# Kernel tuning notes

Measured on AMD Instinct MI355X. Metric: run time of the kernel, lower is better.

## Reference

```python
import jax, jax.numpy as jnp
import numpy as np
import math

N_QUBITS = 6
N_LAYERS = 3
OUT_DIM = 8
B = 131072
F = 24


def _gate_rx(a):
    # RX(a) = [[cos(a/2), -i sin(a/2)], [-i sin(a/2), cos(a/2)]]; a: scalar or [B]
    c = jnp.cos(a / 2).astype(jnp.complex64)
    s = (-1j * jnp.sin(a / 2)).astype(jnp.complex64)
    return jnp.stack([jnp.stack([c, s], -1), jnp.stack([s, c], -1)], -2)


def _gate_ry(a):
    c = jnp.cos(a / 2).astype(jnp.complex64)
    s = jnp.sin(a / 2).astype(jnp.complex64)
    return jnp.stack([jnp.stack([c, -s], -1), jnp.stack([s, c], -1)], -2)


def _gate_rz(a):
    # RZ(a) = diag(e^{-ia/2}, e^{ia/2})
    e = jnp.exp(-0.5j * a.astype(jnp.complex64))
    z = jnp.zeros_like(e)
    return jnp.stack([jnp.stack([e, z], -1), jnp.stack([z, jnp.conj(e)], -1)], -2)


def _apply_1q(state, gate, q, batched):
    # state: [B] + [2]*N_QUBITS ; gate: [2,2] or [B,2,2]
    s = jnp.moveaxis(state, 1 + q, 1)
    if batched:
        out = jnp.einsum('bij,bj...->bi...', gate, s)
    else:
        out = jnp.einsum('ij,bj...->bi...', gate, s)
    return jnp.moveaxis(out, 1, 1 + q)


def _apply_cnot(state, c, t):
    # flip target where control bit == 1
    cax = 1 + c
    s0 = jnp.take(state, 0, axis=cax)
    s1 = jnp.take(state, 1, axis=cax)
    tax = 1 + t if t < c else t  # control axis removed
    s1 = jnp.flip(s1, axis=tax)
    return jnp.stack([s0, s1], axis=cax)


def _circuit(x, theta):
    Bn = x.shape[0]
    # pooling branch of forward: chunks of size ceil(F/n_qubits)=4, mean each
    x_packed = x.reshape(Bn, N_QUBITS, F // N_QUBITS).mean(-1)
    angles = jnp.clip(x_packed, -6.0, 6.0) / 6.0 * math.pi  # [B, n_qubits]

    state = jnp.zeros((Bn,) + (2,) * N_QUBITS, dtype=jnp.complex64)
    state = state.at[(slice(None),) + (0,) * N_QUBITS].set(1.0)

    # angle encoding: RX(a_q), RZ(0.5*a_q) per qubit (batched gates)
    for q in range(N_QUBITS):
        state = _apply_1q(state, _gate_rx(angles[:, q]), q, batched=True)
        state = _apply_1q(state, _gate_rz(0.5 * angles[:, q]), q, batched=True)

    for l in range(N_LAYERS):
        for q in range(N_QUBITS - 1):
            state = _apply_cnot(state, q, q + 1)
        state = _apply_cnot(state, N_QUBITS - 1, 0)
        for q in range(N_QUBITS):
            state = _apply_1q(state, _gate_rx(theta[l, q, 0]), q, batched=False)
            state = _apply_1q(state, _gate_ry(theta[l, q, 1]), q, batched=False)
            state = _apply_1q(state, _gate_rz(theta[l, q, 2]), q, batched=False)

    probs = jnp.abs(state) ** 2  # real
    meas = []
    for k in range(OUT_DIM):
        q = k % N_QUBITS
        if k % 2 == 0:  # PauliZ
            pq = jnp.sum(probs, axis=tuple(a for a in range(1, N_QUBITS + 1) if a != 1 + q))
            meas.append(pq[:, 0] - pq[:, 1])
        else:  # PauliX: Re <psi| X_q |psi>
            flipped = jnp.flip(state, axis=1 + q)
            meas.append(jnp.real(jnp.sum(jnp.conj(state) * flipped, axis=tuple(range(1, N_QUBITS + 1)))))
    return jnp.stack(meas, axis=1).astype(jnp.float32)  # [B, out_dim]


def setup_inputs() -> dict:
    key = jax.random.key(0)
    k1, k2 = jax.random.split(key)
    x = jax.random.normal(k1, (B, F), dtype=jnp.float32)
    theta = jax.random.normal(k2, (N_LAYERS, N_QUBITS, 3), dtype=jnp.float32) * 0.1
    return {"x": x, "theta": theta}


def reference(x, theta):
    return _circuit(x, theta)
```

## Files before the change

### kernel.cpp

```cpp
#include <hip/hip_runtime.h>
#include <math.h>


struct cf { float r, i; };

__device__ __forceinline__ cf cmul(cf a, cf b) {
    return { fmaf(a.r, b.r, -a.i * b.i), fmaf(a.r, b.i, a.i * b.r) };
}
__device__ __forceinline__ cf cmac(cf acc, cf g, cf v) {
    acc.r = fmaf(g.r, v.r, fmaf(-g.i, v.i, acc.r));
    acc.i = fmaf(g.r, v.i, fmaf(g.i, v.r, acc.i));
    return acc;
}

constexpr int DPP_X1  = 0xB1;
constexpr int DPP_X2  = 0x4E;
constexpr int DPP_C01 = 0xB4;

template<int CTRL>
__device__ __forceinline__ float dppf(float v) {
    return __int_as_float(__builtin_amdgcn_mov_dpp(__float_as_int(v), CTRL, 0xF, 0xF, true));
}
template<int CTRL>
__device__ __forceinline__ cf dppc(cf v) { return { dppf<CTRL>(v.r), dppf<CTRL>(v.i) }; }

template<int M>
__device__ __forceinline__ void apply1q(cf* st, cf g00, cf g01, cf g10, cf g11) {
#pragma unroll
    for (int i = 0; i < 16; ++i) {
        if (i & M) continue;
        cf a = st[i], b = st[i + M];
        cf na = cmul(g00, a); na = cmac(na, g01, b);
        cf nb = cmul(g10, a); nb = cmac(nb, g11, b);
        st[i] = na; st[i + M] = nb;
    }
}

template<int XCTRL>
__device__ __forceinline__ void apply1q_lane(cf* st, bool hi, cf g00, cf g01, cf g10, cf g11) {
    cf ga, gb;
    ga.r = hi ? g11.r : g00.r;  ga.i = hi ? g11.i : g00.i;
    gb.r = hi ? g10.r : g01.r;  gb.i = hi ? g10.i : g01.i;
#pragma unroll
    for (int i = 0; i < 16; ++i) {
        cf part = dppc<XCTRL>(st[i]);
        cf n = cmul(ga, st[i]);
        n = cmac(n, gb, part);
        st[i] = n;
    }
}

template<int MC, int MT>
__device__ __forceinline__ void cnot_local(cf* st) {
#pragma unroll
    for (int i = 0; i < 16; ++i) {
        if ((i & MC) && !(i & MT)) { cf t = st[i]; st[i] = st[i + MT]; st[i + MT] = t; }
    }
}

__global__ __launch_bounds__(256, 4) void qsim_kernel(
    const float* __restrict__ x, const float* __restrict__ theta,
    float* __restrict__ out) {
    __shared__ float gs[18 * 8];
    const int t = threadIdx.x;
    if (t < 18) {
        const float* th = theta + t * 3;
        float sx, cx, sy, cy, sz, cz;
        __sincosf(0.5f * th[0], &sx, &cx);
        __sincosf(0.5f * th[1], &sy, &cy);
        __sincosf(0.5f * th[2], &sz, &cz);
        cf m00 = {  cy * cx,  sy * sx };
        cf m01 = { -sy * cx, -cy * sx };
        cf m10 = {  sy * cx, -cy * sx };
        cf m11 = {  cy * cx, -sy * sx };
        cf e0 = { cz, -sz }, e1 = { cz, sz };
        cf g00 = cmul(e0, m00), g01 = cmul(e0, m01);
        cf g10 = cmul(e1, m10), g11 = cmul(e1, m11);
        float* o = gs + t * 8;
        o[0] = g00.r; o[1] = g00.i; o[2] = g01.r; o[3] = g01.i;
        o[4] = g10.r; o[5] = g10.i; o[6] = g11.r; o[7] = g11.i;
    }
    __syncthreads();

    const int g = blockIdx.x * 256 + t;
    const int e = g >> 2;
    const int p = g & 3;
    const bool l1 = (p & 2) != 0;
    const bool l0 = (p & 1) != 0;

    const float4* xv = reinterpret_cast<const float4*>(x + (size_t)e * 24);
    cf v0[6], v1[6];
#pragma unroll
    for (int q = 0; q < 6; ++q) {
        float4 xq = xv[q];
        float m = (xq.x + xq.y + xq.z + xq.w) * 0.25f;
        m = fminf(fmaxf(m, -6.0f), 6.0f);
        float a = m * 0.52359877559829887308f;
        float s2, c2, s4, c4;
        __sincosf(0.50f * a, &s2, &c2);
        __sincosf(0.25f * a, &s4, &c4);
        v0[q] = { c4 * c2, -s4 * c2 };
        v1[q] = { s4 * s2, -c4 * s2 };
    }

    cf f0, f1;
    f0.r = l1 ? v1[0].r : v0[0].r;  f0.i = l1 ? v1[0].i : v0[0].i;
    f1.r = l0 ? v1[1].r : v0[1].r;  f1.i = l0 ? v1[1].i : v0[1].i;

    cf st[16];
    st[0] = cmul(f0, f1);
#pragma unroll
    for (int q = 2; q < 6; ++q) {
        const int m = 8 >> (q - 2);
#pragma unroll
        for (int i = 0; i < 16; i += 2 * m) {
            st[i + m] = cmul(st[i], v1[q]);
            st[i]     = cmul(st[i], v0[q]);
        }
    }

#pragma unroll 1
    for (int l = 0; l < 3; ++l) {
#pragma unroll
        for (int i = 0; i < 16; ++i) st[i] = dppc<DPP_C01>(st[i]);
#pragma unroll
        for (int i = 0; i < 8; ++i) {
            cf lo = st[i], hi = st[i + 8];
            st[i].r     = l0 ? hi.r : lo.r;  st[i].i     = l0 ? hi.i : lo.i;
            st[i + 8].r = l0 ? lo.r : hi.r;  st[i + 8].i = l0 ? lo.i : hi.i;
        }
        cnot_local<8, 4>(st);
        cnot_local<4, 2>(st);
        cnot_local<2, 1>(st);
#pragma unroll
        for (int i = 1; i < 16; i += 2) st[i] = dppc<DPP_X2>(st[i]);

        const float* gg = gs + l * 48;
#define G4(k) cf{gg[8*(k)+0], gg[8*(k)+1]}, cf{gg[8*(k)+2], gg[8*(k)+3]}, \
              cf{gg[8*(k)+4], gg[8*(k)+5]}, cf{gg[8*(k)+6], gg[8*(k)+7]}
        apply1q_lane<DPP_X2>(st, l1, G4(0));
        apply1q_lane<DPP_X1>(st, l0, G4(1));
        apply1q<8>(st, G4(2));
        apply1q<4>(st, G4(3));
        apply1q<2>(st, G4(4));
        apply1q<1>(st, G4(5));
#undef G4
    }

    float z0 = 0.f, z2 = 0.f, z4 = 0.f, x1s = 0.f, x3s = 0.f, x5s = 0.f;
#pragma unroll
    for (int i = 0; i < 16; ++i) {
        float pr = fmaf(st[i].r, st[i].r, st[i].i * st[i].i);
        z0 += pr;
        z2 = (i & 8) ? z2 - pr : z2 + pr;
        z4 = (i & 2) ? z4 - pr : z4 + pr;
        cf part = dppc<DPP_X1>(st[i]);
        x1s = fmaf(st[i].r, part.r, fmaf(st[i].i, part.i, x1s));
    }
    if (l1) z0 = -z0;
#pragma unroll
    for (int i = 0; i < 16; ++i) {
        if (!(i & 4)) x3s = fmaf(st[i].r, st[i + 4].r, fmaf(st[i].i, st[i + 4].i, x3s));
        if (!(i & 1)) x5s = fmaf(st[i].r, st[i + 1].r, fmaf(st[i].i, st[i + 1].i, x5s));
    }
    x3s *= 2.f; x5s *= 2.f;

    z0  += dppf<DPP_X1>(z0);   z0  += dppf<DPP_X2>(z0);
    z2  += dppf<DPP_X1>(z2);   z2  += dppf<DPP_X2>(z2);
    z4  += dppf<DPP_X1>(z4);   z4  += dppf<DPP_X2>(z4);
    x1s += dppf<DPP_X1>(x1s);  x1s += dppf<DPP_X2>(x1s);
    x3s += dppf<DPP_X1>(x3s);  x3s += dppf<DPP_X2>(x3s);
    x5s += dppf<DPP_X1>(x5s);  x5s += dppf<DPP_X2>(x5s);

    float o0 = l1 ? (l0 ? x3s : z2) : (l0 ? x1s : z0);
    float o1 = l1 ? (l0 ? x1s : z0) : (l0 ? x5s : z4);
    out[(size_t)e * 8 + p] = o0;
    out[(size_t)e * 8 + 4 + p] = o1;
}

extern "C" void kernel_launch(void* const* d_in, const int* in_sizes, int n_in,
                              void* d_out, int out_size, void* d_ws, size_t ws_size,
                              hipStream_t stream) {
    const float* x     = (const float*)d_in[0];
    const float* theta = (const float*)d_in[1];
    float* out = (float*)d_out;
    const int B = in_sizes[0] / 24;
    const int threads = B * 4;
    qsim_kernel<<<dim3(threads / 256), dim3(256), 0, stream>>>(x, theta, out);
}
```

Baseline: 89.97 us.

## Precompute circuit unitary in bf16 and apply it per sample with MFMA

```diff
diff --git a/kernel.cpp b/kernel.cpp
--- a/kernel.cpp
+++ b/kernel.cpp
@@ -13,6 +13,9 @@
     return acc;
 }
 
+typedef short short8 __attribute__((ext_vector_type(8)));
+typedef float f32x4 __attribute__((ext_vector_type(4)));
+
 constexpr int DPP_X1  = 0xB1;
 constexpr int DPP_X2  = 0x4E;
 constexpr int DPP_C01 = 0xB4;
@@ -23,6 +26,10 @@
 }
 template<int CTRL>
 __device__ __forceinline__ cf dppc(cf v) { return { dppf<CTRL>(v.r), dppf<CTRL>(v.i) }; }
+
+__device__ __forceinline__ unsigned pkbf(float lo, float hi) {
+    return __builtin_amdgcn_perm(__float_as_uint(hi), __float_as_uint(lo), 0x07060302u);
+}
 
 template<int M>
 __device__ __forceinline__ void apply1q(cf* st, cf g00, cf g01, cf g10, cf g11) {
@@ -35,7 +42,6 @@
         st[i] = na; st[i + M] = nb;
     }
 }
-
 template<int XCTRL>
 __device__ __forceinline__ void apply1q_lane(cf* st, bool hi, cf g00, cf g01, cf g10, cf g11) {
     cf ga, gb;
@@ -49,7 +55,6 @@
         st[i] = n;
     }
 }
-
 template<int MC, int MT>
 __device__ __forceinline__ void cnot_local(cf* st) {
 #pragma unroll
@@ -58,9 +63,8 @@
     }
 }
 
-__global__ __launch_bounds__(256, 4) void qsim_kernel(
-    const float* __restrict__ x, const float* __restrict__ theta,
-    float* __restrict__ out) {
+__global__ void ubuild_kernel(const float* __restrict__ theta,
+                              unsigned short* __restrict__ W) {
     __shared__ float gs[18 * 8];
     const int t = threadIdx.x;
     if (t < 18) {
@@ -82,42 +86,15 @@
     }
     __syncthreads();
 
-    const int g = blockIdx.x * 256 + t;
-    const int e = g >> 2;
-    const int p = g & 3;
+    const int k = t >> 2;
+    const int p = t & 3;
     const bool l1 = (p & 2) != 0;
     const bool l0 = (p & 1) != 0;
 
-    const float4* xv = reinterpret_cast<const float4*>(x + (size_t)e * 24);
-    cf v0[6], v1[6];
-#pragma unroll
-    for (int q = 0; q < 6; ++q) {
-        float4 xq = xv[q];
-        float m = (xq.x + xq.y + xq.z + xq.w) * 0.25f;
-        m = fminf(fmaxf(m, -6.0f), 6.0f);
-        float a = m * 0.52359877559829887308f;
-        float s2, c2, s4, c4;
-        __sincosf(0.50f * a, &s2, &c2);
-        __sincosf(0.25f * a, &s4, &c4);
-        v0[q] = { c4 * c2, -s4 * c2 };
-        v1[q] = { s4 * s2, -c4 * s2 };
-    }
-
-    cf f0, f1;
-    f0.r = l1 ? v1[0].r : v0[0].r;  f0.i = l1 ? v1[0].i : v0[0].i;
-    f1.r = l0 ? v1[1].r : v0[1].r;  f1.i = l0 ? v1[1].i : v0[1].i;
-
     cf st[16];
-    st[0] = cmul(f0, f1);
-#pragma unroll
-    for (int q = 2; q < 6; ++q) {
-        const int m = 8 >> (q - 2);
-#pragma unroll
-        for (int i = 0; i < 16; i += 2 * m) {
-            st[i + m] = cmul(st[i], v1[q]);
-            st[i]     = cmul(st[i], v0[q]);
-        }
-    }
+#pragma unroll
+    for (int i = 0; i < 16; ++i) st[i] = { 0.f, 0.f };
+    if ((k >> 4) == p) st[k & 15] = { 1.f, 0.f };
 
 #pragma unroll 1
     for (int l = 0; l < 3; ++l) {
@@ -136,8 +113,8 @@
         for (int i = 1; i < 16; i += 2) st[i] = dppc<DPP_X2>(st[i]);
 
         const float* gg = gs + l * 48;
-#define G4(k) cf{gg[8*(k)+0], gg[8*(k)+1]}, cf{gg[8*(k)+2], gg[8*(k)+3]}, \
-              cf{gg[8*(k)+4], gg[8*(k)+5]}, cf{gg[8*(k)+6], gg[8*(k)+7]}
+#define G4(kk) cf{gg[8*(kk)+0], gg[8*(kk)+1]}, cf{gg[8*(kk)+2], gg[8*(kk)+3]}, \
+               cf{gg[8*(kk)+4], gg[8*(kk)+5]}, cf{gg[8*(kk)+6], gg[8*(kk)+7]}
         apply1q_lane<DPP_X2>(st, l1, G4(0));
         apply1q_lane<DPP_X1>(st, l0, G4(1));
         apply1q<8>(st, G4(2));
@@ -147,35 +124,152 @@
 #undef G4
     }
 
-    float z0 = 0.f, z2 = 0.f, z4 = 0.f, x1s = 0.f, x3s = 0.f, x5s = 0.f;
-#pragma unroll
-    for (int i = 0; i < 16; ++i) {
-        float pr = fmaf(st[i].r, st[i].r, st[i].i * st[i].i);
-        z0 += pr;
-        z2 = (i & 8) ? z2 - pr : z2 + pr;
-        z4 = (i & 2) ? z4 - pr : z4 + pr;
-        cf part = dppc<DPP_X1>(st[i]);
-        x1s = fmaf(st[i].r, part.r, fmaf(st[i].i, part.i, x1s));
-    }
-    if (l1) z0 = -z0;
-#pragma unroll
-    for (int i = 0; i < 16; ++i) {
-        if (!(i & 4)) x3s = fmaf(st[i].r, st[i + 4].r, fmaf(st[i].i, st[i + 4].i, x3s));
-        if (!(i & 1)) x5s = fmaf(st[i].r, st[i + 1].r, fmaf(st[i].i, st[i + 1].i, x5s));
-    }
-    x3s *= 2.f; x5s *= 2.f;
-
-    z0  += dppf<DPP_X1>(z0);   z0  += dppf<DPP_X2>(z0);
-    z2  += dppf<DPP_X1>(z2);   z2  += dppf<DPP_X2>(z2);
-    z4  += dppf<DPP_X1>(z4);   z4  += dppf<DPP_X2>(z4);
-    x1s += dppf<DPP_X1>(x1s);  x1s += dppf<DPP_X2>(x1s);
-    x3s += dppf<DPP_X1>(x3s);  x3s += dppf<DPP_X2>(x3s);
-    x5s += dppf<DPP_X1>(x5s);  x5s += dppf<DPP_X2>(x5s);
-
-    float o0 = l1 ? (l0 ? x3s : z2) : (l0 ? x1s : z0);
-    float o1 = l1 ? (l0 ? x1s : z0) : (l0 ? x5s : z4);
-    out[(size_t)e * 8 + p] = o0;
-    out[(size_t)e * 8 + 4 + p] = o1;
+#pragma unroll
+    for (int i = 0; i < 16; ++i) {
+        const int n = (p << 4) | i;
+        unsigned ur = __float_as_uint(st[i].r); ur = (ur + 0x7FFFu + ((ur >> 16) & 1u)) >> 16;
+        unsigned ui = __float_as_uint(st[i].i); ui = (ui + 0x7FFFu + ((ui >> 16) & 1u)) >> 16;
+        W[n * 72 + k]        = (unsigned short)ur;
+        W[4608 + n * 72 + k] = (unsigned short)ui;
+    }
+}
+
+__global__ __launch_bounds__(256, 3) void qmain_kernel(
+    const float* __restrict__ x, const unsigned short* __restrict__ W,
+    float* __restrict__ out) {
+    __shared__ unsigned short Wr[64 * 72];
+    __shared__ unsigned short Wi[64 * 72];
+    __shared__ float sc[4][16 * 132];
+    const int t = threadIdx.x;
+    {
+        const unsigned* src = (const unsigned*)W;
+        unsigned* dr = (unsigned*)Wr; unsigned* di = (unsigned*)Wi;
+#pragma unroll 1
+        for (int i = t; i < 2304; i += 256) { dr[i] = src[i]; di[i] = src[2304 + i]; }
+    }
+    __syncthreads();
+
+    const int wave = t >> 6, lane = t & 63;
+    const int l = lane & 15, c2 = lane >> 4;
+    float* scb = sc[wave];
+
+#pragma unroll 1
+    for (int tt = 0; tt < 2; ++tt) {
+        const int tile = (blockIdx.x * 4 + wave) * 2 + tt;
+        const int E = tile << 4;
+
+        const int e = E + l;
+        const float4* xv = (const float4*)(x + (size_t)e * 24);
+        cf v0[6], v1[6];
+#pragma unroll
+        for (int q = 0; q < 6; ++q) {
+            float4 xq = xv[q];
+            float m = (xq.x + xq.y + xq.z + xq.w) * 0.25f;
+            m = fminf(fmaxf(m, -6.f), 6.f);
+            float a = m * 0.52359877559829887308f;
+            float s2, c2v, s4, c4;
+            __sincosf(0.50f * a, &s2, &c2v);
+            __sincosf(0.25f * a, &s4, &c4);
+            v0[q] = { c4 * c2v, -s4 * c2v };
+            v1[q] = { s4 * s2, -c4 * s2 };
+        }
+        cf t34[4];
+        t34[0] = cmul(v0[3], v0[4]); t34[1] = cmul(v0[3], v1[4]);
+        t34[2] = cmul(v1[3], v0[4]); t34[3] = cmul(v1[3], v1[4]);
+        cf w8[8];
+#pragma unroll
+        for (int a2 = 0; a2 < 4; ++a2) {
+            w8[2 * a2]     = cmul(t34[a2], v0[5]);
+            w8[2 * a2 + 1] = cmul(t34[a2], v1[5]);
+        }
+        cf f1 = (c2 & 2) ? v1[1] : v0[1];
+        cf f2 = (c2 & 1) ? v1[2] : v0[2];
+        cf pc = cmul(f1, f2);
+        cf p0 = cmul(v0[0], pc), p1 = cmul(v1[0], pc);
+        float ar0f[8], ai0f[8], ar1f[8], ai1f[8];
+#pragma unroll
+        for (int j = 0; j < 8; ++j) {
+            cf a0 = cmul(p0, w8[j]); cf a1 = cmul(p1, w8[j]);
+            ar0f[j] = a0.r; ai0f[j] = a0.i; ar1f[j] = a1.r; ai1f[j] = a1.i;
+        }
+        union U8 { short8 v; unsigned u[4]; };
+        U8 ar0, ai0, ar1, ai1;
+#pragma unroll
+        for (int d = 0; d < 4; ++d) {
+            ar0.u[d] = pkbf(ar0f[2 * d], ar0f[2 * d + 1]);
+            ai0.u[d] = pkbf(ai0f[2 * d], ai0f[2 * d + 1]);
+            ar1.u[d] = pkbf(ar1f[2 * d], ar1f[2 * d + 1]);
+            ai1.u[d] = pkbf(ai1f[2 * d], ai1f[2 * d + 1]);
+        }
+
+#pragma unroll
+        for (int nt = 0; nt < 4; ++nt) {
+            const unsigned short* rbr = &Wr[(nt * 16 + l) * 72 + c2 * 8];
+            const unsigned short* rbi = &Wi[(nt * 16 + l) * 72 + c2 * 8];
+            short8 br0 = *(const short8*)rbr;
+            short8 br1 = *(const short8*)(rbr + 32);
+            short8 bi0 = *(const short8*)rbi;
+            short8 bi1 = *(const short8*)(rbi + 32);
+            f32x4 z = { 0.f, 0.f, 0.f, 0.f };
+            f32x4 rp = __builtin_amdgcn_mfma_f32_16x16x32_bf16(ar0.v, br0, z, 0, 0, 0);
+            rp = __builtin_amdgcn_mfma_f32_16x16x32_bf16(ar1.v, br1, rp, 0, 0, 0);
+            f32x4 rm = __builtin_amdgcn_mfma_f32_16x16x32_bf16(ai0.v, bi0, z, 0, 0, 0);
+            rm = __builtin_amdgcn_mfma_f32_16x16x32_bf16(ai1.v, bi1, rm, 0, 0, 0);
+            f32x4 ci = __builtin_amdgcn_mfma_f32_16x16x32_bf16(ar0.v, bi0, z, 0, 0, 0);
+            ci = __builtin_amdgcn_mfma_f32_16x16x32_bf16(ar1.v, bi1, ci, 0, 0, 0);
+            ci = __builtin_amdgcn_mfma_f32_16x16x32_bf16(ai0.v, br0, ci, 0, 0, 0);
+            ci = __builtin_amdgcn_mfma_f32_16x16x32_bf16(ai1.v, br1, ci, 0, 0, 0);
+#pragma unroll
+            for (int rg = 0; rg < 4; ++rg) {
+                const int el = c2 * 4 + rg;
+                const int n = nt * 16 + l;
+                float2 val = make_float2(rp[rg] - rm[rg], ci[rg]);
+                *(float2*)&scb[el * 132 + n * 2] = val;
+            }
+        }
+
+        const int q = lane & 3, el2 = lane >> 2;
+        const float* sr = &scb[el2 * 132 + q * 32];
+        cf s[16];
+#pragma unroll
+        for (int j = 0; j < 8; ++j) {
+            f32x4 ld = *(const f32x4*)&sr[j * 4];
+            s[2 * j]     = { ld[0], ld[1] };
+            s[2 * j + 1] = { ld[2], ld[3] };
+        }
+        float p_all = 0.f, p_b3 = 0.f, p_b1 = 0.f;
+#pragma unroll
+        for (int j = 0; j < 16; ++j) {
+            float pp = fmaf(s[j].r, s[j].r, s[j].i * s[j].i);
+            p_all += pp;
+            if (j & 8) p_b3 += pp;
+            if (j & 2) p_b1 += pp;
+        }
+        float z2p = p_all - 2.f * p_b3;
+        float z4p = p_all - 2.f * p_b1;
+        float z0p = (q & 2) ? -p_all : p_all;
+        float x1p = 0.f, x3p = 0.f, x5p = 0.f;
+#pragma unroll
+        for (int j = 0; j < 16; ++j) {
+            float prr = dppf<DPP_X1>(s[j].r);
+            float pii = dppf<DPP_X1>(s[j].i);
+            x1p = fmaf(s[j].r, prr, fmaf(s[j].i, pii, x1p));
+            x3p = fmaf(s[j].r, s[j ^ 4].r, fmaf(s[j].i, s[j ^ 4].i, x3p));
+            x5p = fmaf(s[j].r, s[j ^ 1].r, fmaf(s[j].i, s[j ^ 1].i, x5p));
+        }
+        z0p += dppf<DPP_X1>(z0p);  z0p += dppf<DPP_X2>(z0p);
+        z2p += dppf<DPP_X1>(z2p);  z2p += dppf<DPP_X2>(z2p);
+        z4p += dppf<DPP_X1>(z4p);  z4p += dppf<DPP_X2>(z4p);
+        x1p += dppf<DPP_X1>(x1p);  x1p += dppf<DPP_X2>(x1p);
+        x3p += dppf<DPP_X1>(x3p);  x3p += dppf<DPP_X2>(x3p);
+        x5p += dppf<DPP_X1>(x5p);  x5p += dppf<DPP_X2>(x5p);
+
+        float oa = (q == 0) ? z0p : (q == 1) ? x1p : (q == 2) ? z2p : x3p;
+        float ob = (q == 0) ? z4p : (q == 1) ? x5p : (q == 2) ? z0p : x1p;
+        const size_t obase = (size_t)(E + el2) * 8;
+        out[obase + q]     = oa;
+        out[obase + 4 + q] = ob;
+    }
 }
 
 extern "C" void kernel_launch(void* const* d_in, const int* in_sizes, int n_in,
@@ -185,6 +279,8 @@
     const float* theta = (const float*)d_in[1];
     float* out = (float*)d_out;
     const int B = in_sizes[0] / 24;
-    const int threads = B * 4;
-    qsim_kernel<<<dim3(threads / 256), dim3(256), 0, stream>>>(x, theta, out);
-}
+    unsigned short* W = (unsigned short*)d_ws;
+    ubuild_kernel<<<1, 256, 0, stream>>>(theta, W);
+    const int tiles = B / 16;
+    qmain_kernel<<<tiles / 8, 256, 0, stream>>>(x, W, out);
+}
```

Result: slower. 93.95 us (+4.4%).
